# Kernel tuning notes

Hardware: AMD Instinct MI355X
Metric: run time of the kernel (lower is better)

## Reference

```python
import jax, jax.numpy as jnp
import numpy as np

TEMPERATURE = 0.5  # init temperature; attn_drop=0.0 so dropout is identity


def setup_inputs() -> dict:
    key = jax.random.key(0)
    k1, k2, k3 = jax.random.split(key, 3)
    B, H, N, D = 4, 8, 2048, 64
    q = jax.random.normal(k1, (B, H, N, D), dtype=jnp.float32)
    k = jax.random.normal(k2, (B, H, N, D), dtype=jnp.float32)
    v = jax.random.normal(k3, (B, H, N, D), dtype=jnp.float32)
    scale = jnp.asarray(D ** -0.5, dtype=jnp.float32)
    return {"q": q, "k": k, "v": v, "scale": scale}


def reference(q, k, v, scale):
    # logits: [B,H,N,N]
    logits = jnp.einsum("bhqd,bhkd->bhqk", q, k) * scale
    # first softmax acts as a soft mask over keys
    soft_mask = jax.nn.softmax(logits / TEMPERATURE, axis=-1)
    # second softmax over masked logits (elementwise product, NOT matmul)
    attn = jax.nn.softmax(logits * soft_mask, axis=-1)
    # dropout with p=0.0 is identity
    out = jnp.einsum("bhqk,bhkd->bhqd", attn, v)
    return out
```

## Files before the change

kernel.cpp:

```cpp
#include <hip/hip_runtime.h>


typedef _Float16 f16;
typedef f16 f16x8 __attribute__((ext_vector_type(8)));
typedef f16 f16x4 __attribute__((ext_vector_type(4)));
typedef float f32x4 __attribute__((ext_vector_type(4)));

#define MFMA32(a, b, c) __builtin_amdgcn_mfma_f32_16x16x32_f16((a), (b), (c), 0, 0, 0)
#define MFMA16(a, b, c) __builtin_amdgcn_mfma_f32_16x16x16f16((a), (b), (c), 0, 0, 0)
#define EXP2(x) __builtin_amdgcn_exp2f(x)

#define N_CTX 2048
#define DH 64
#define KT 64
#define NKT (N_CTX / KT)
#define ROWS 64
#define QS 72

#define C2 2.885390081777927f

__device__ inline unsigned pk(float a, float b) {
    typedef __fp16 fp16x2_t __attribute__((ext_vector_type(2)));
    union { fp16x2_t v; unsigned u; } x;
    x.v = __builtin_amdgcn_cvt_pkrtz(a, b);
    return x.u;
}

__global__ __launch_bounds__(256, 4)
void stk_attn_mfma(const float* __restrict__ qg, const float* __restrict__ kg,
                   const float* __restrict__ vglob, const float* __restrict__ sg,
                   float* __restrict__ og) {
    __shared__ f16 Ks[2][KT * QS];
    __shared__ f16 Vt[2][DH * QS];

    const int tid  = threadIdx.x;
    const int wv   = tid >> 6;
    const int lane = tid & 63;
    const int l15  = lane & 15;
    const int q4   = lane >> 4;
    const int vp   = tid & 31;
    const int vgr  = tid >> 5;
    const int bh   = blockIdx.x & 31;
    const int q0   = (blockIdx.x >> 5) * ROWS;
    const float scale2 = sg[0] * C2;

    const float* qb = qg + (size_t)bh * N_CTX * DH;
    const float* kb = kg + (size_t)bh * N_CTX * DH;
    const float* vb = vglob + (size_t)bh * N_CTX * DH;
    float*       ob = og + (size_t)bh * N_CTX * DH;

    f16x8 aq[2];
    {
        const float* qrow = qb + (size_t)(q0 + wv * 16 + l15) * DH;
        #pragma unroll
        for (int kc = 0; kc < 2; ++kc) {
            float4 a0 = *(const float4*)&qrow[kc * 32 + q4 * 8];
            float4 a1 = *(const float4*)&qrow[kc * 32 + q4 * 8 + 4];
            union { f16x8 h; unsigned u[4]; } A;
            A.u[0] = pk(a0.x * scale2, a0.y * scale2);
            A.u[1] = pk(a0.z * scale2, a0.w * scale2);
            A.u[2] = pk(a1.x * scale2, a1.y * scale2);
            A.u[3] = pk(a1.z * scale2, a1.w * scale2);
            aq[kc] = A.h;
        }
    }

    f16* const ks_w  = &Ks[0][0];
    const f16* const ks_r = &Ks[0][l15 * QS + q4 * 8];
    f16* const vt_w  = &Vt[0][(vgr * 8) * QS + 2 * vp];
    const f16* const vt_r = &Vt[0][l15 * QS + q4 * 4];
    const int KSB = KT * QS;

    float s1 = 0.f;
    float4 kr[4];
    #pragma unroll
    for (int it = 0; it < 4; ++it) {
        int idx = it * 256 + tid;
        kr[it] = *(const float4*)&kb[((size_t)(idx >> 4)) * DH + (idx & 15) * 4];
    }
    #pragma unroll
    for (int it = 0; it < 4; ++it) {
        int idx = it * 256 + tid;
        *(uint2*)&ks_w[(idx >> 4) * QS + (idx & 15) * 4] =
            make_uint2(pk(kr[it].x, kr[it].y), pk(kr[it].z, kr[it].w));
    }
    #pragma unroll
    for (int it = 0; it < 4; ++it) {
        int idx = it * 256 + tid;
        kr[it] = *(const float4*)&kb[((size_t)KT + (idx >> 4)) * DH + (idx & 15) * 4];
    }
    __syncthreads();

    for (int kt = 0; kt < NKT; ++kt) {
        const int cur = (kt & 1) * KSB, nxt = KSB - cur;
        #pragma unroll
        for (int it = 0; it < 4; ++it) {
            int idx = it * 256 + tid;
            *(uint2*)&ks_w[nxt + (idx >> 4) * QS + (idx & 15) * 4] =
                make_uint2(pk(kr[it].x, kr[it].y), pk(kr[it].z, kr[it].w));
        }
        {
            int tn = (kt + 2 < NKT) ? kt + 2 : NKT - 1;
            #pragma unroll
            for (int it = 0; it < 4; ++it) {
                int idx = it * 256 + tid;
                kr[it] = *(const float4*)&kb[((size_t)tn * KT + (idx >> 4)) * DH + (idx & 15) * 4];
            }
        }
        #pragma unroll
        for (int kgi = 0; kgi < 4; ++kgi) {
            f16x8 b0 = *(const f16x8*)&ks_r[cur + kgi * 16 * QS];
            f16x8 b1 = *(const f16x8*)&ks_r[cur + kgi * 16 * QS + 32];
            f32x4 acc = {0.f, 0.f, 0.f, 0.f};
            acc = MFMA32(b0, aq[0], acc);
            acc = MFMA32(b1, aq[1], acc);
            s1 += EXP2(acc[0]);
            s1 += EXP2(acc[1]);
            s1 += EXP2(acc[2]);
            s1 += EXP2(acc[3]);
        }
        __syncthreads();
    }
    s1 += __shfl_xor(s1, 16, 64);
    s1 += __shfl_xor(s1, 32, 64);
    const float inv1 = 0.5f / s1;

    float l2 = 0.f;
    f32x4 O[4];
    #pragma unroll
    for (int dt = 0; dt < 4; ++dt) O[dt] = (f32x4){0.f, 0.f, 0.f, 0.f};

    float4 vr0, vr1, vr2, vr3;
    #pragma unroll
    for (int it = 0; it < 4; ++it) {
        int idx = it * 256 + tid;
        kr[it] = *(const float4*)&kb[((size_t)(idx >> 4)) * DH + (idx & 15) * 4];
    }
    #pragma unroll
    for (int it = 0; it < 4; ++it) {
        int idx = it * 256 + tid;
        *(uint2*)&ks_w[(idx >> 4) * QS + (idx & 15) * 4] =
            make_uint2(pk(kr[it].x, kr[it].y), pk(kr[it].z, kr[it].w));
    }
    {
        const float* vs = vb + ((size_t)(2 * vp)) * DH + vgr * 8;
        float4 a0 = *(const float4*)(vs);
        float4 a1 = *(const float4*)(vs + 4);
        float4 b0 = *(const float4*)(vs + DH);
        float4 b1 = *(const float4*)(vs + DH + 4);
        #pragma unroll
        for (int j = 0; j < 4; ++j) {
            *(unsigned*)&vt_w[j * QS] = pk(((const float*)&a0)[j], ((const float*)&b0)[j]);
            *(unsigned*)&vt_w[(4 + j) * QS] = pk(((const float*)&a1)[j], ((const float*)&b1)[j]);
        }
        const float* vs1 = vb + ((size_t)(KT + 2 * vp)) * DH + vgr * 8;
        vr0 = *(const float4*)(vs1);
        vr1 = *(const float4*)(vs1 + 4);
        vr2 = *(const float4*)(vs1 + DH);
        vr3 = *(const float4*)(vs1 + DH + 4);
    }
    #pragma unroll
    for (int it = 0; it < 4; ++it) {
        int idx = it * 256 + tid;
        kr[it] = *(const float4*)&kb[((size_t)KT + (idx >> 4)) * DH + (idx & 15) * 4];
    }
    __syncthreads();

    for (int kt = 0; kt < NKT; ++kt) {
        const int cur = (kt & 1) * KSB, nxt = KSB - cur;
        #pragma unroll
        for (int it = 0; it < 4; ++it) {
            int idx = it * 256 + tid;
            *(uint2*)&ks_w[nxt + (idx >> 4) * QS + (idx & 15) * 4] =
                make_uint2(pk(kr[it].x, kr[it].y), pk(kr[it].z, kr[it].w));
        }
        #pragma unroll
        for (int j = 0; j < 4; ++j) {
            *(unsigned*)&vt_w[nxt + j * QS] = pk(((const float*)&vr0)[j], ((const float*)&vr2)[j]);
            *(unsigned*)&vt_w[nxt + (4 + j) * QS] = pk(((const float*)&vr1)[j], ((const float*)&vr3)[j]);
        }
        f16x4 pfr[4];
        #pragma unroll
        for (int kgi = 0; kgi < 4; ++kgi) {
            f16x8 b0 = *(const f16x8*)&ks_r[cur + kgi * 16 * QS];
            f16x8 b1 = *(const f16x8*)&ks_r[cur + kgi * 16 * QS + 32];
            f32x4 acc = {0.f, 0.f, 0.f, 0.f};
            acc = MFMA32(b0, aq[0], acc);
            acc = MFMA32(b1, aq[1], acc);
            float e2r[4];
            #pragma unroll
            for (int r = 0; r < 4; ++r) {
                float a  = acc[r];
                float e1 = EXP2(a);
                float e2 = EXP2((a * e1) * inv1);
                l2 += e2;
                e2r[r] = e2;
            }
            union { f16x4 h; unsigned u[2]; } P;
            P.u[0] = pk(e2r[0], e2r[1]);
            P.u[1] = pk(e2r[2], e2r[3]);
            pfr[kgi] = P.h;
        }
        {
            int tn = (kt + 2 < NKT) ? kt + 2 : NKT - 1;
            #pragma unroll
            for (int it = 0; it < 4; ++it) {
                int idx = it * 256 + tid;
                kr[it] = *(const float4*)&kb[((size_t)tn * KT + (idx >> 4)) * DH + (idx & 15) * 4];
            }
            const float* vs = vb + ((size_t)tn * KT + 2 * vp) * DH + vgr * 8;
            vr0 = *(const float4*)(vs);
            vr1 = *(const float4*)(vs + 4);
            vr2 = *(const float4*)(vs + DH);
            vr3 = *(const float4*)(vs + DH + 4);
        }
        #pragma unroll
        for (int kgi = 0; kgi < 4; ++kgi) {
            #pragma unroll
            for (int dt = 0; dt < 4; ++dt) {
                f16x4 av = *(const f16x4*)&vt_r[cur + dt * 16 * QS + kgi * 16];
                O[dt] = MFMA16(av, pfr[kgi], O[dt]);
            }
        }
        __syncthreads();
    }

    l2 += __shfl_xor(l2, 16, 64);
    l2 += __shfl_xor(l2, 32, 64);
    const float invl2 = 1.0f / l2;
    const size_t orow = (size_t)(q0 + wv * 16 + l15) * DH;
    #pragma unroll
    for (int dt = 0; dt < 4; ++dt) {
        float4 o;
        o.x = O[dt][0] * invl2;
        o.y = O[dt][1] * invl2;
        o.z = O[dt][2] * invl2;
        o.w = O[dt][3] * invl2;
        *(float4*)&ob[orow + dt * 16 + q4 * 4] = o;
    }
}

extern "C" void kernel_launch(void* const* d_in, const int* in_sizes, int n_in,
                              void* d_out, int out_size, void* d_ws, size_t ws_size,
                              hipStream_t stream) {
    const float* q = (const float*)d_in[0];
    const float* k = (const float*)d_in[1];
    const float* v = (const float*)d_in[2];
    const float* s = (const float*)d_in[3];
    float* out = (float*)d_out;
    dim3 grid(32 * 32);
    stk_attn_mfma<<<grid, 256, 0, stream>>>(q, k, v, s, out);
}
```

Before: 196.0 us.

## Double block and key tile sizes, compute row sum with MFMA ones-vector

Blocks grow to 512 threads covering 128 query rows, and key/value tiles grow to 128 keys. Each staged K/V tile is therefore reused by twice as many rows, halving the number of loop iterations and global K/V loads per query. The second-softmax denominator is now accumulated by an extra MFMA against a ones vector instead of scalar adds and shuffles, and the prefetch is moved ahead of the compute loop. The risks are fewer blocks in the grid (512), higher LDS use, and slightly different rounding because the row sums are taken from fp16 values.

After: 175.1 us. 1.12x faster.

```diff
diff --git a/kernel.cpp b/kernel.cpp
--- a/kernel.cpp
+++ b/kernel.cpp
@@ -12,10 +12,14 @@
 
 #define N_CTX 2048
 #define DH 64
-#define KT 64
+#define KT 128
 #define NKT (N_CTX / KT)
-#define ROWS 64
+#define ROWS 128
 #define QS 72
+#define VS 136
+#define KSB (KT * QS)
+#define VSB (DH * VS)
+#define LDS_BYTES ((2 * KSB + 2 * VSB) * 2)
 
 #define C2 2.885390081777927f
 
@@ -26,20 +30,19 @@
     return x.u;
 }
 
-__global__ __launch_bounds__(256, 4)
+__global__ __launch_bounds__(512, 4)
 void stk_attn_mfma(const float* __restrict__ qg, const float* __restrict__ kg,
                    const float* __restrict__ vglob, const float* __restrict__ sg,
                    float* __restrict__ og) {
-    __shared__ f16 Ks[2][KT * QS];
-    __shared__ f16 Vt[2][DH * QS];
+    extern __shared__ f16 smem[];
+    f16* const KsB = smem;
+    f16* const VtB = smem + 2 * KSB;
 
     const int tid  = threadIdx.x;
     const int wv   = tid >> 6;
     const int lane = tid & 63;
     const int l15  = lane & 15;
     const int q4   = lane >> 4;
-    const int vp   = tid & 31;
-    const int vgr  = tid >> 5;
     const int bh   = blockIdx.x & 31;
     const int q0   = (blockIdx.x >> 5) * ROWS;
     const float scale2 = sg[0] * C2;
@@ -65,52 +68,51 @@
         }
     }
 
-    f16* const ks_w  = &Ks[0][0];
-    const f16* const ks_r = &Ks[0][l15 * QS + q4 * 8];
-    f16* const vt_w  = &Vt[0][(vgr * 8) * QS + 2 * vp];
-    const f16* const vt_r = &Vt[0][l15 * QS + q4 * 4];
-    const int KSB = KT * QS;
+    f16* const ks_w  = KsB;
+    const f16* const ks_r = KsB + l15 * QS + q4 * 8;
+    f16* const vt_w  = VtB + (wv * 8) * VS + 2 * lane;
+    const f16* const vt_r = VtB + l15 * VS + q4 * 4;
 
     float s1 = 0.f;
     float4 kr[4];
     #pragma unroll
     for (int it = 0; it < 4; ++it) {
-        int idx = it * 256 + tid;
+        int idx = it * 512 + tid;
         kr[it] = *(const float4*)&kb[((size_t)(idx >> 4)) * DH + (idx & 15) * 4];
     }
     #pragma unroll
     for (int it = 0; it < 4; ++it) {
-        int idx = it * 256 + tid;
+        int idx = it * 512 + tid;
         *(uint2*)&ks_w[(idx >> 4) * QS + (idx & 15) * 4] =
             make_uint2(pk(kr[it].x, kr[it].y), pk(kr[it].z, kr[it].w));
     }
     #pragma unroll
     for (int it = 0; it < 4; ++it) {
-        int idx = it * 256 + tid;
+        int idx = it * 512 + tid;
         kr[it] = *(const float4*)&kb[((size_t)KT + (idx >> 4)) * DH + (idx & 15) * 4];
     }
     __syncthreads();
 
     for (int kt = 0; kt < NKT; ++kt) {
-        const int cur = (kt & 1) * KSB, nxt = KSB - cur;
+        const int curK = (kt & 1) * KSB, nxtK = KSB - curK;
         #pragma unroll
         for (int it = 0; it < 4; ++it) {
-            int idx = it * 256 + tid;
-            *(uint2*)&ks_w[nxt + (idx >> 4) * QS + (idx & 15) * 4] =
+            int idx = it * 512 + tid;
+            *(uint2*)&ks_w[nxtK + (idx >> 4) * QS + (idx & 15) * 4] =
                 make_uint2(pk(kr[it].x, kr[it].y), pk(kr[it].z, kr[it].w));
         }
         {
             int tn = (kt + 2 < NKT) ? kt + 2 : NKT - 1;
             #pragma unroll
             for (int it = 0; it < 4; ++it) {
-                int idx = it * 256 + tid;
+                int idx = it * 512 + tid;
                 kr[it] = *(const float4*)&kb[((size_t)tn * KT + (idx >> 4)) * DH + (idx & 15) * 4];
             }
         }
         #pragma unroll
-        for (int kgi = 0; kgi < 4; ++kgi) {
-            f16x8 b0 = *(const f16x8*)&ks_r[cur + kgi * 16 * QS];
-            f16x8 b1 = *(const f16x8*)&ks_r[cur + kgi * 16 * QS + 32];
+        for (int kgi = 0; kgi < 8; ++kgi) {
+            f16x8 b0 = *(const f16x8*)&ks_r[curK + kgi * 16 * QS];
+            f16x8 b1 = *(const f16x8*)&ks_r[curK + kgi * 16 * QS + 32];
             f32x4 acc = {0.f, 0.f, 0.f, 0.f};
             acc = MFMA32(b0, aq[0], acc);
             acc = MFMA32(b1, aq[1], acc);
@@ -125,35 +127,36 @@
     s1 += __shfl_xor(s1, 32, 64);
     const float inv1 = 0.5f / s1;
 
-    float l2 = 0.f;
     f32x4 O[4];
     #pragma unroll
     for (int dt = 0; dt < 4; ++dt) O[dt] = (f32x4){0.f, 0.f, 0.f, 0.f};
+    f32x4 Oe = {0.f, 0.f, 0.f, 0.f};
+    const f16x4 ones = {(f16)1.f, (f16)1.f, (f16)1.f, (f16)1.f};
 
     float4 vr0, vr1, vr2, vr3;
     #pragma unroll
     for (int it = 0; it < 4; ++it) {
-        int idx = it * 256 + tid;
+        int idx = it * 512 + tid;
         kr[it] = *(const float4*)&kb[((size_t)(idx >> 4)) * DH + (idx & 15) * 4];
     }
     #pragma unroll
     for (int it = 0; it < 4; ++it) {
-        int idx = it * 256 + tid;
+        int idx = it * 512 + tid;
         *(uint2*)&ks_w[(idx >> 4) * QS + (idx & 15) * 4] =
             make_uint2(pk(kr[it].x, kr[it].y), pk(kr[it].z, kr[it].w));
     }
     {
-        const float* vs = vb + ((size_t)(2 * vp)) * DH + vgr * 8;
+        const float* vs = vb + ((size_t)(2 * lane)) * DH + wv * 8;
         float4 a0 = *(const float4*)(vs);
         float4 a1 = *(const float4*)(vs + 4);
         float4 b0 = *(const float4*)(vs + DH);
         float4 b1 = *(const float4*)(vs + DH + 4);
         #pragma unroll
         for (int j = 0; j < 4; ++j) {
-            *(unsigned*)&vt_w[j * QS] = pk(((const float*)&a0)[j], ((const float*)&b0)[j]);
-            *(unsigned*)&vt_w[(4 + j) * QS] = pk(((const float*)&a1)[j], ((const float*)&b1)[j]);
-        }
-        const float* vs1 = vb + ((size_t)(KT + 2 * vp)) * DH + vgr * 8;
+            *(unsigned*)&vt_w[j * VS] = pk(((const float*)&a0)[j], ((const float*)&b0)[j]);
+            *(unsigned*)&vt_w[(4 + j) * VS] = pk(((const float*)&a1)[j], ((const float*)&b1)[j]);
+        }
+        const float* vs1 = vb + ((size_t)(KT + 2 * lane)) * DH + wv * 8;
         vr0 = *(const float4*)(vs1);
         vr1 = *(const float4*)(vs1 + 4);
         vr2 = *(const float4*)(vs1 + DH);
@@ -161,29 +164,42 @@
     }
     #pragma unroll
     for (int it = 0; it < 4; ++it) {
-        int idx = it * 256 + tid;
+        int idx = it * 512 + tid;
         kr[it] = *(const float4*)&kb[((size_t)KT + (idx >> 4)) * DH + (idx & 15) * 4];
     }
     __syncthreads();
 
     for (int kt = 0; kt < NKT; ++kt) {
-        const int cur = (kt & 1) * KSB, nxt = KSB - cur;
+        const int curK = (kt & 1) * KSB, nxtK = KSB - curK;
+        const int curV = (kt & 1) * VSB, nxtV = VSB - curV;
         #pragma unroll
         for (int it = 0; it < 4; ++it) {
-            int idx = it * 256 + tid;
-            *(uint2*)&ks_w[nxt + (idx >> 4) * QS + (idx & 15) * 4] =
+            int idx = it * 512 + tid;
+            *(uint2*)&ks_w[nxtK + (idx >> 4) * QS + (idx & 15) * 4] =
                 make_uint2(pk(kr[it].x, kr[it].y), pk(kr[it].z, kr[it].w));
         }
         #pragma unroll
         for (int j = 0; j < 4; ++j) {
-            *(unsigned*)&vt_w[nxt + j * QS] = pk(((const float*)&vr0)[j], ((const float*)&vr2)[j]);
-            *(unsigned*)&vt_w[nxt + (4 + j) * QS] = pk(((const float*)&vr1)[j], ((const float*)&vr3)[j]);
-        }
-        f16x4 pfr[4];
-        #pragma unroll
-        for (int kgi = 0; kgi < 4; ++kgi) {
-            f16x8 b0 = *(const f16x8*)&ks_r[cur + kgi * 16 * QS];
-            f16x8 b1 = *(const f16x8*)&ks_r[cur + kgi * 16 * QS + 32];
+            *(unsigned*)&vt_w[nxtV + j * VS] = pk(((const float*)&vr0)[j], ((const float*)&vr2)[j]);
+            *(unsigned*)&vt_w[nxtV + (4 + j) * VS] = pk(((const float*)&vr1)[j], ((const float*)&vr3)[j]);
+        }
+        {
+            int tn = (kt + 2 < NKT) ? kt + 2 : NKT - 1;
+            #pragma unroll
+            for (int it = 0; it < 4; ++it) {
+                int idx = it * 512 + tid;
+                kr[it] = *(const float4*)&kb[((size_t)tn * KT + (idx >> 4)) * DH + (idx & 15) * 4];
+            }
+            const float* vs = vb + ((size_t)(tn * KT + 2 * lane)) * DH + wv * 8;
+            vr0 = *(const float4*)(vs);
+            vr1 = *(const float4*)(vs + 4);
+            vr2 = *(const float4*)(vs + DH);
+            vr3 = *(const float4*)(vs + DH + 4);
+        }
+        #pragma unroll
+        for (int kgi = 0; kgi < 8; ++kgi) {
+            f16x8 b0 = *(const f16x8*)&ks_r[curK + kgi * 16 * QS];
+            f16x8 b1 = *(const f16x8*)&ks_r[curK + kgi * 16 * QS + 32];
             f32x4 acc = {0.f, 0.f, 0.f, 0.f};
             acc = MFMA32(b0, aq[0], acc);
             acc = MFMA32(b1, aq[1], acc);
@@ -192,42 +208,23 @@
             for (int r = 0; r < 4; ++r) {
                 float a  = acc[r];
                 float e1 = EXP2(a);
-                float e2 = EXP2((a * e1) * inv1);
-                l2 += e2;
-                e2r[r] = e2;
+                e2r[r] = EXP2((a * e1) * inv1);
             }
             union { f16x4 h; unsigned u[2]; } P;
             P.u[0] = pk(e2r[0], e2r[1]);
             P.u[1] = pk(e2r[2], e2r[3]);
-            pfr[kgi] = P.h;
-        }
-        {
-            int tn = (kt + 2 < NKT) ? kt + 2 : NKT - 1;
-            #pragma unroll
-            for (int it = 0; it < 4; ++it) {
-                int idx = it * 256 + tid;
-                kr[it] = *(const float4*)&kb[((size_t)tn * KT + (idx >> 4)) * DH + (idx & 15) * 4];
-            }
-            const float* vs = vb + ((size_t)tn * KT + 2 * vp) * DH + vgr * 8;
-            vr0 = *(const float4*)(vs);
-            vr1 = *(const float4*)(vs + 4);
-            vr2 = *(const float4*)(vs + DH);
-            vr3 = *(const float4*)(vs + DH + 4);
-        }
-        #pragma unroll
-        for (int kgi = 0; kgi < 4; ++kgi) {
+            f16x4 pfr = P.h;
+            Oe = MFMA16(ones, pfr, Oe);
             #pragma unroll
             for (int dt = 0; dt < 4; ++dt) {
-                f16x4 av = *(const f16x4*)&vt_r[cur + dt * 16 * QS + kgi * 16];
-                O[dt] = MFMA16(av, pfr[kgi], O[dt]);
+                f16x4 av = *(const f16x4*)&vt_r[curV + dt * 16 * VS + kgi * 16];
+                O[dt] = MFMA16(av, pfr, O[dt]);
             }
         }
         __syncthreads();
     }
 
-    l2 += __shfl_xor(l2, 16, 64);
-    l2 += __shfl_xor(l2, 32, 64);
-    const float invl2 = 1.0f / l2;
+    const float invl2 = 1.0f / Oe[0];
     const size_t orow = (size_t)(q0 + wv * 16 + l15) * DH;
     #pragma unroll
     for (int dt = 0; dt < 4; ++dt) {
@@ -248,6 +245,6 @@
     const float* v = (const float*)d_in[2];
     const float* s = (const float*)d_in[3];
     float* out = (float*)d_out;
-    dim3 grid(32 * 32);
-    stk_attn_mfma<<<grid, 256, 0, stream>>>(q, k, v, s, out);
+    dim3 grid(32 * 16);
+    stk_attn_mfma<<<grid, 512, LDS_BYTES, stream>>>(q, k, v, s, out);
 }
```
